# Kernel tuning notes

Hardware: AMD Instinct MI355X
Metric: run time of the kernel (lower is better)

## Reference

```python
import jax, jax.numpy as jnp
import numpy as np

NEG_SLOPE = 0.2


def gat_conv(x, edge_index, W, a_src, a_dst, b, concat):
    """PyG-style GATConv: add self-loops, linear, edge attention, scatter-softmax, scatter-add."""
    N = x.shape[0]
    H, C = a_src.shape
    loop = jnp.arange(N)
    src = jnp.concatenate([edge_index[0], loop])  # source j (messages flow j -> i)
    dst = jnp.concatenate([edge_index[1], loop])  # target i (aggregation node)
    h = (x @ W).reshape(N, H, C)                  # [N,H,C]
    alpha_s = jnp.sum(h * a_src, axis=-1)         # [N,H]
    alpha_d = jnp.sum(h * a_dst, axis=-1)         # [N,H]
    e = jax.nn.leaky_relu(alpha_s[src] + alpha_d[dst], NEG_SLOPE)  # [E,H]
    # numerically stable scatter-softmax over edges grouped by destination node
    m = jax.ops.segment_max(e, dst, num_segments=N)                # [N,H]
    ex = jnp.exp(e - m[dst])
    denom = jax.ops.segment_sum(ex, dst, num_segments=N)           # [N,H]
    alpha = ex / (denom[dst] + 1e-16)                              # [E,H]
    out = jax.ops.segment_sum(h[src] * alpha[:, :, None], dst, num_segments=N)  # [N,H,C]
    out = out.reshape(N, H * C) if concat else out.mean(axis=1)
    return out + b


def setup_inputs() -> dict:
    key = jax.random.key(0)
    ks = jax.random.split(key, 12)
    N, E, F_IN, HID, OUT, HEADS = 100000, 1600000, 128, 128, 64, 4
    C1 = HID // HEADS
    x = jax.random.normal(ks[0], (N, F_IN), dtype=jnp.float32)
    edge_index = jax.random.randint(ks[1], (2, E), 0, N, dtype=jnp.int64)
    s = 0.05
    return {
        "x": x,
        "edge_index": edge_index,
        "W1": jax.random.normal(ks[2], (F_IN, HEADS * C1), dtype=jnp.float32) * s,
        "a_src1": jax.random.normal(ks[3], (HEADS, C1), dtype=jnp.float32) * s,
        "a_dst1": jax.random.normal(ks[4], (HEADS, C1), dtype=jnp.float32) * s,
        "b1": jnp.zeros((HEADS * C1,), dtype=jnp.float32),
        "W2": jax.random.normal(ks[5], (HID, OUT), dtype=jnp.float32) * s,
        "a_src2": jax.random.normal(ks[6], (1, OUT), dtype=jnp.float32) * s,
        "a_dst2": jax.random.normal(ks[7], (1, OUT), dtype=jnp.float32) * s,
        "b2": jnp.zeros((OUT,), dtype=jnp.float32),
    }


def reference(x, edge_index, W1, a_src1, a_dst1, b1, W2, a_src2, a_dst2, b2):
    h = jax.nn.elu(gat_conv(x, edge_index, W1, a_src1, a_dst1, b1, concat=True))
    # F.dropout(p=0.5, training=False) is the identity in eval mode
    out = gat_conv(h, edge_index, W2, a_src2, a_dst2, b2, concat=False)
    return out
```

## Files before the change

kernel.cpp:

```cpp
#include <hip/hip_runtime.h>
#include <hip/hip_fp16.h>
#include <math.h>


#define BSH 9
#define DPB 512
#define NBK 256
#define CH1 16384
#define LOG2E 1.44269504088896f

__device__ __forceinline__ float exp2_fast(float x) {
#if __has_builtin(__builtin_amdgcn_exp2f)
    return __builtin_amdgcn_exp2f(x);
#else
    return exp2f(x);
#endif
}


__global__ __launch_bounds__(256) void bucket_hist(const int* __restrict__ ei, int E, int N,
                                                   unsigned* __restrict__ bcount) {
    __shared__ unsigned hist[NBK];
    int t = threadIdx.x;
    hist[t] = 0;
    __syncthreads();
    int Etot = E + N;
    for (int k = blockIdx.x * 256 + t; k < Etot; k += gridDim.x * 256) {
        int d = (k < E) ? ei[E + k] : (k - E);
        atomicAdd(&hist[d >> BSH], 1u);
    }
    __syncthreads();
    unsigned c = hist[t];
    if (c) atomicAdd(&bcount[t], c);
}

__global__ void scan_buckets(const unsigned* __restrict__ bcount, unsigned* __restrict__ bbase,
                             unsigned* __restrict__ bcursor) {
    __shared__ unsigned s[NBK];
    int t = threadIdx.x;
    unsigned v = bcount[t];
    s[t] = v;
    __syncthreads();
    for (int o = 1; o < NBK; o <<= 1) {
        unsigned add = (t >= o) ? s[t - o] : 0;
        __syncthreads();
        s[t] += add;
        __syncthreads();
    }
    unsigned excl = s[t] - v;
    bbase[t] = excl;
    bcursor[t] = excl;
    if (t == NBK - 1) bbase[NBK] = excl + v;
}

__global__ __launch_bounds__(256) void bucket_scatter(const int* __restrict__ ei, int E, int N,
                                                      unsigned* __restrict__ bcursor,
                                                      uint2* __restrict__ rec) {
    __shared__ unsigned hist[NBK];
    __shared__ unsigned base[NBK];
    int t = threadIdx.x;
    hist[t] = 0;
    __syncthreads();
    int Etot = E + N;
    int k0 = blockIdx.x * CH1;
    int k1 = min(k0 + CH1, Etot);
    for (int k = k0 + t; k < k1; k += 256) {
        int d = (k < E) ? ei[E + k] : (k - E);
        atomicAdd(&hist[d >> BSH], 1u);
    }
    __syncthreads();
    unsigned c = hist[t];
    base[t] = c ? atomicAdd(&bcursor[t], c) : 0u;
    hist[t] = 0;
    __syncthreads();
    for (int k = k0 + t; k < k1; k += 256) {
        int s, d;
        if (k < E) { s = ei[k]; d = ei[E + k]; } else { s = d = k - E; }
        int b = d >> BSH;
        unsigned r = atomicAdd(&hist[b], 1u);
        rec[base[b] + r] = make_uint2((unsigned)s, (unsigned)d);
    }
}

__global__ __launch_bounds__(256) void bucket_sort(const uint2* __restrict__ rec,
                                                   const unsigned* __restrict__ bbase,
                                                   int* __restrict__ offs, int* __restrict__ srcs,
                                                   int N, int Etot) {
    __shared__ unsigned hist[DPB];
    __shared__ unsigned tsum[256];
    int t = threadIdx.x, bb = blockIdx.x;
    unsigned r0 = bbase[bb], r1 = bbase[bb + 1];
    hist[t] = 0;
    hist[t + 256] = 0;
    __syncthreads();
    int dlo = bb << BSH;
    for (unsigned k = r0 + t; k < r1; k += 256) {
        uint2 e = rec[k];
        atomicAdd(&hist[e.y - dlo], 1u);
    }
    __syncthreads();
    unsigned h0 = hist[2 * t], h1 = hist[2 * t + 1];
    tsum[t] = h0 + h1;
    __syncthreads();
    for (int o = 1; o < 256; o <<= 1) {
        unsigned a = (t >= o) ? tsum[t - o] : 0;
        __syncthreads();
        tsum[t] += a;
        __syncthreads();
    }
    unsigned tb = tsum[t] - (h0 + h1);
    int d0 = dlo + 2 * t;
    if (d0 < N) offs[d0] = (int)(r0 + tb);
    if (d0 + 1 < N) offs[d0 + 1] = (int)(r0 + tb + h0);
    hist[2 * t] = tb;
    hist[2 * t + 1] = tb + h0;
    __syncthreads();
    for (unsigned k = r0 + t; k < r1; k += 256) {
        uint2 e = rec[k];
        unsigned r = atomicAdd(&hist[e.y - dlo], 1u);
        srcs[r0 + r] = (int)e.x;
    }
    if (bb == 0 && t == 0) offs[N] = Etot;
}


template <int NC, int H, typename InT, typename OutT>
__global__ __launch_bounds__(256) void gemm_k128(const InT* __restrict__ A,
                                                 const float* __restrict__ B,
                                                 OutT* __restrict__ C,
                                                 const float* __restrict__ a_src,
                                                 const float* __restrict__ a_dst,
                                                 float* __restrict__ as,
                                                 float* __restrict__ ad, int M) {
    constexpr int BM = 64, BK = 32, K = 128;
    constexpr int TPR = NC / 4;
    constexpr int R = BM / (256 / TPR);
    constexpr int TXH = TPR / H;
    __shared__ float AsT[BK][BM + 4];
    __shared__ float Bs[BK][NC];
    int tid = threadIdx.x;
    int tx = tid % TPR, ty = tid / TPR;
    int rowBase = blockIdx.x * BM;
    float acc[R][4] = {};
    for (int k0 = 0; k0 < K; k0 += BK) {
#pragma unroll
        for (int i = 0; i < 4; ++i) {
            int lin = tid + i * 256;
            int row = lin >> 4;
            int kp = lin & 15;
            int grow = rowBase + row;
            if (grow >= M) grow = M - 1;
            float2 v;
            if constexpr (sizeof(InT) == 2) {
                __half2 hv = *reinterpret_cast<const __half2*>((const __half*)A + (size_t)grow * K + k0 + kp * 2);
                v = __half22float2(hv);
            } else {
                v = *reinterpret_cast<const float2*>((const float*)A + (size_t)grow * K + k0 + kp * 2);
            }
            AsT[kp * 2][row] = v.x;
            AsT[kp * 2 + 1][row] = v.y;
        }
#pragma unroll
        for (int i = 0; i < (BK * NC) / 1024; ++i) {
            int lin = tid + i * 256;
            int row = lin / (NC / 4);
            int col4 = lin % (NC / 4);
            float4 v = *reinterpret_cast<const float4*>(B + (size_t)(k0 + row) * NC + col4 * 4);
            *reinterpret_cast<float4*>(&Bs[row][col4 * 4]) = v;
        }
        __syncthreads();
#pragma unroll
        for (int kk = 0; kk < BK; ++kk) {
            float4 bv = *reinterpret_cast<const float4*>(&Bs[kk][tx * 4]);
            float a[R];
#pragma unroll
            for (int r4 = 0; r4 < R; r4 += 4) {
                float4 av = *reinterpret_cast<const float4*>(&AsT[kk][ty * R + r4]);
                a[r4] = av.x; a[r4 + 1] = av.y; a[r4 + 2] = av.z; a[r4 + 3] = av.w;
            }
#pragma unroll
            for (int r = 0; r < R; ++r) {
                acc[r][0] = fmaf(a[r], bv.x, acc[r][0]);
                acc[r][1] = fmaf(a[r], bv.y, acc[r][1]);
                acc[r][2] = fmaf(a[r], bv.z, acc[r][2]);
                acc[r][3] = fmaf(a[r], bv.w, acc[r][3]);
            }
        }
        __syncthreads();
    }
    float4 asv = *reinterpret_cast<const float4*>(a_src + tx * 4);
    float4 adv = *reinterpret_cast<const float4*>(a_dst + tx * 4);
#pragma unroll
    for (int r = 0; r < R; ++r) {
        int grow = rowBase + ty * R + r;
        bool live = grow < M;
        if (live) {
            if constexpr (sizeof(OutT) == 2) {
                __half2 p0 = __floats2half2_rn(acc[r][0], acc[r][1]);
                __half2 p1 = __floats2half2_rn(acc[r][2], acc[r][3]);
                __half2* cp = reinterpret_cast<__half2*>((__half*)C + (size_t)grow * NC + tx * 4);
                cp[0] = p0;
                cp[1] = p1;
            } else {
                float4 v = make_float4(acc[r][0], acc[r][1], acc[r][2], acc[r][3]);
                *reinterpret_cast<float4*>((float*)C + (size_t)grow * NC + tx * 4) = v;
            }
        }
        float ps = acc[r][0] * asv.x + acc[r][1] * asv.y + acc[r][2] * asv.z + acc[r][3] * asv.w;
        float pd = acc[r][0] * adv.x + acc[r][1] * adv.y + acc[r][2] * adv.z + acc[r][3] * adv.w;
#pragma unroll
        for (int o = 1; o < TXH; o <<= 1) {
            ps += __shfl_xor(ps, o, 64);
            pd += __shfl_xor(pd, o, 64);
        }
        if ((tx & (TXH - 1)) == 0 && live) {
            int head = tx / TXH;
            as[(size_t)grow * H + head] = ps * LOG2E;
            ad[(size_t)grow * H + head] = pd * LOG2E;
        }
    }
}


__global__ __launch_bounds__(256) void aggregate1(const __half* __restrict__ h,
                                                  const float* __restrict__ as,
                                                  const float* __restrict__ ad,
                                                  const int* __restrict__ offs,
                                                  const int* __restrict__ srcs,
                                                  const float* __restrict__ bias,
                                                  __half* __restrict__ out, int N) {
    unsigned wid = (blockIdx.x * blockDim.x + threadIdx.x) >> 6;
    unsigned lane = threadIdx.x & 63;
    if (wid >= (unsigned)N) return;
    unsigned head = lane >> 4;
    float adv = ad[wid * 4u + head];
    int e0 = offs[wid], e1 = offs[wid + 1];
    int e1m1 = e1 - 1;
    const __half2* hp = reinterpret_cast<const __half2*>(h);
    float acc0 = 0.f, acc1 = 0.f, den = 0.f;
    for (int e = e0; e < e1; e += 4) {
        unsigned j0 = (unsigned)srcs[min(e, e1m1)];
        unsigned j1 = (unsigned)srcs[min(e + 1, e1m1)];
        unsigned j2 = (unsigned)srcs[min(e + 2, e1m1)];
        unsigned j3 = (unsigned)srcs[min(e + 3, e1m1)];
        float t0 = as[j0 * 4u + head] + adv;
        float t1 = as[j1 * 4u + head] + adv;
        float t2 = as[j2 * 4u + head] + adv;
        float t3 = as[j3 * 4u + head] + adv;
        __half2 h0 = hp[j0 * 64u + lane];
        __half2 h1 = hp[j1 * 64u + lane];
        __half2 h2 = hp[j2 * 64u + lane];
        __half2 h3 = hp[j3 * 64u + lane];
        float x0 = exp2_fast(fmaxf(t0, 0.2f * t0));
        float x1 = exp2_fast(fmaxf(t1, 0.2f * t1));
        float x2 = exp2_fast(fmaxf(t2, 0.2f * t2));
        float x3 = exp2_fast(fmaxf(t3, 0.2f * t3));
        x1 = (e + 1 < e1) ? x1 : 0.f;
        x2 = (e + 2 < e1) ? x2 : 0.f;
        x3 = (e + 3 < e1) ? x3 : 0.f;
        float2 f0 = __half22float2(h0), f1 = __half22float2(h1);
        float2 f2 = __half22float2(h2), f3 = __half22float2(h3);
        acc0 = fmaf(x0, f0.x, acc0); acc1 = fmaf(x0, f0.y, acc1);
        acc0 = fmaf(x1, f1.x, acc0); acc1 = fmaf(x1, f1.y, acc1);
        acc0 = fmaf(x2, f2.x, acc0); acc1 = fmaf(x2, f2.y, acc1);
        acc0 = fmaf(x3, f3.x, acc0); acc1 = fmaf(x3, f3.y, acc1);
        den += (x0 + x1) + (x2 + x3);
    }
    float r = 1.0f / (den + 1e-16f);
    float v0 = acc0 * r + bias[2 * lane];
    float v1 = acc1 * r + bias[2 * lane + 1];
    v0 = (v0 > 0.f) ? v0 : expm1f(v0);
    v1 = (v1 > 0.f) ? v1 : expm1f(v1);
    reinterpret_cast<__half2*>(out)[wid * 64u + lane] = __floats2half2_rn(v0, v1);
}

__global__ __launch_bounds__(256) void aggregate2(const __half* __restrict__ h,
                                                  const float* __restrict__ as,
                                                  const float* __restrict__ ad,
                                                  const int* __restrict__ offs,
                                                  const int* __restrict__ srcs,
                                                  const float* __restrict__ bias,
                                                  float* __restrict__ out, int N) {
    unsigned wid = (blockIdx.x * blockDim.x + threadIdx.x) >> 6;
    unsigned lane = threadIdx.x & 63;
    if (wid >= (unsigned)N) return;
    float adv = ad[wid];
    int e0 = offs[wid], e1 = offs[wid + 1];
    int e1m1 = e1 - 1;
    float acc = 0.f, den = 0.f;
    for (int e = e0; e < e1; e += 4) {
        unsigned j0 = (unsigned)srcs[min(e, e1m1)];
        unsigned j1 = (unsigned)srcs[min(e + 1, e1m1)];
        unsigned j2 = (unsigned)srcs[min(e + 2, e1m1)];
        unsigned j3 = (unsigned)srcs[min(e + 3, e1m1)];
        float t0 = as[j0] + adv;
        float t1 = as[j1] + adv;
        float t2 = as[j2] + adv;
        float t3 = as[j3] + adv;
        __half h0 = h[j0 * 64u + lane];
        __half h1 = h[j1 * 64u + lane];
        __half h2 = h[j2 * 64u + lane];
        __half h3 = h[j3 * 64u + lane];
        float x0 = exp2_fast(fmaxf(t0, 0.2f * t0));
        float x1 = exp2_fast(fmaxf(t1, 0.2f * t1));
        float x2 = exp2_fast(fmaxf(t2, 0.2f * t2));
        float x3 = exp2_fast(fmaxf(t3, 0.2f * t3));
        x1 = (e + 1 < e1) ? x1 : 0.f;
        x2 = (e + 2 < e1) ? x2 : 0.f;
        x3 = (e + 3 < e1) ? x3 : 0.f;
        acc = fmaf(x0, __half2float(h0), acc);
        acc = fmaf(x1, __half2float(h1), acc);
        acc = fmaf(x2, __half2float(h2), acc);
        acc = fmaf(x3, __half2float(h3), acc);
        den += (x0 + x1) + (x2 + x3);
    }
    float r = 1.0f / (den + 1e-16f);
    out[wid * 64u + lane] = acc * r + bias[lane];
}


extern "C" void kernel_launch(void* const* d_in, const int* in_sizes, int n_in,
                              void* d_out, int out_size, void* d_ws, size_t ws_size,
                              hipStream_t stream) {
    const float* x      = (const float*)d_in[0];
    const int*   ei     = (const int*)d_in[1];
    const float* W1     = (const float*)d_in[2];
    const float* a_src1 = (const float*)d_in[3];
    const float* a_dst1 = (const float*)d_in[4];
    const float* b1     = (const float*)d_in[5];
    const float* W2     = (const float*)d_in[6];
    const float* a_src2 = (const float*)d_in[7];
    const float* a_dst2 = (const float*)d_in[8];
    const float* b2     = (const float*)d_in[9];
    float* out = (float*)d_out;

    const int N = out_size / 64;
    const int E = in_sizes[1] / 2;
    const int Etot = E + N;

    size_t off = 0;
    auto carve = [&](size_t bytes) -> void* {
        void* p = (char*)d_ws + off;
        off += (bytes + 255) & ~(size_t)255;
        return p;
    };
    __half* h1      = (__half*)carve((size_t)N * 128 * 2);
    __half* hmid    = (__half*)carve((size_t)N * 128 * 2);
    float* as1      = (float*)carve((size_t)N * 4 * 4);
    float* ad1      = (float*)carve((size_t)N * 4 * 4);
    float* as2      = (float*)carve((size_t)N * 4);
    float* ad2      = (float*)carve((size_t)N * 4);
    int*   offs     = (int*)carve((size_t)(N + 1) * 4);
    int*   srcs     = (int*)carve((size_t)Etot * 4);
    uint2* rec      = (uint2*)carve((size_t)Etot * 8);
    unsigned* bcount  = (unsigned*)carve(NBK * 4);
    unsigned* bbase   = (unsigned*)carve((NBK + 1) * 4);
    unsigned* bcursor = (unsigned*)carve(NBK * 4);
    __half* h2      = h1;

    hipMemsetAsync(bcount, 0, NBK * sizeof(unsigned), stream);
    bucket_hist<<<128, 256, 0, stream>>>(ei, E, N, bcount);
    scan_buckets<<<1, 256, 0, stream>>>(bcount, bbase, bcursor);
    bucket_scatter<<<(Etot + CH1 - 1) / CH1, 256, 0, stream>>>(ei, E, N, bcursor, rec);
    bucket_sort<<<(N + DPB - 1) / DPB, 256, 0, stream>>>(rec, bbase, offs, srcs, N, Etot);

    gemm_k128<128, 4, float, __half><<<(N + 63) / 64, 256, 0, stream>>>(
        x, W1, h1, a_src1, a_dst1, as1, ad1, N);
    aggregate1<<<(N + 3) / 4, 256, 0, stream>>>(h1, as1, ad1, offs, srcs, b1, hmid, N);

    gemm_k128<64, 1, __half, __half><<<(N + 63) / 64, 256, 0, stream>>>(
        hmid, W2, h2, a_src2, a_dst2, as2, ad2, N);
    aggregate2<<<(N + 3) / 4, 256, 0, stream>>>(h2, as2, ad2, offs, srcs, b2, out, N);
}
```

Before: 407.6 us.

## Process four destination nodes per wave with wide vector gathers in aggregation

Merges the two aggregation kernels into one templated kernel in which each 16-lane quarter-wave handles one destination node. Each lane loads 16 or 8 bytes of the source feature row and accumulates several channels, in place of one whole wave per node with 2- or 4-byte loads. The aim is fewer, wider memory transactions and more nodes in flight per wave. The cost is load imbalance: every node's loop runs to the maximum degree among the four nodes sharing a wave, and the edge unroll drops from 4 to 2.

```diff
diff --git a/kernel.cpp b/kernel.cpp
--- a/kernel.cpp
+++ b/kernel.cpp
@@ -1,6 +1,7 @@
 #include <hip/hip_runtime.h>
 #include <hip/hip_fp16.h>
 #include <math.h>
+#include <string.h>
 
 
 #define BSH 9
@@ -222,100 +223,104 @@
 }
 
 
-__global__ __launch_bounds__(256) void aggregate1(const __half* __restrict__ h,
+template <int H, int F, bool DOELU, typename OutT>
+__global__ __launch_bounds__(256) void aggregateQ(const __half* __restrict__ h,
                                                   const float* __restrict__ as,
                                                   const float* __restrict__ ad,
                                                   const int* __restrict__ offs,
                                                   const int* __restrict__ srcs,
                                                   const float* __restrict__ bias,
-                                                  __half* __restrict__ out, int N) {
-    unsigned wid = (blockIdx.x * blockDim.x + threadIdx.x) >> 6;
+                                                  OutT* __restrict__ out, int N) {
+    constexpr int CPL = F / 16;
+    constexpr int NH2 = CPL / 2;
+    unsigned wave = (blockIdx.x * blockDim.x + threadIdx.x) >> 6;
     unsigned lane = threadIdx.x & 63;
-    if (wid >= (unsigned)N) return;
-    unsigned head = lane >> 4;
-    float adv = ad[wid * 4u + head];
-    int e0 = offs[wid], e1 = offs[wid + 1];
-    int e1m1 = e1 - 1;
-    const __half2* hp = reinterpret_cast<const __half2*>(h);
-    float acc0 = 0.f, acc1 = 0.f, den = 0.f;
-    for (int e = e0; e < e1; e += 4) {
-        unsigned j0 = (unsigned)srcs[min(e, e1m1)];
-        unsigned j1 = (unsigned)srcs[min(e + 1, e1m1)];
-        unsigned j2 = (unsigned)srcs[min(e + 2, e1m1)];
-        unsigned j3 = (unsigned)srcs[min(e + 3, e1m1)];
-        float t0 = as[j0 * 4u + head] + adv;
-        float t1 = as[j1 * 4u + head] + adv;
-        float t2 = as[j2 * 4u + head] + adv;
-        float t3 = as[j3 * 4u + head] + adv;
-        __half2 h0 = hp[j0 * 64u + lane];
-        __half2 h1 = hp[j1 * 64u + lane];
-        __half2 h2 = hp[j2 * 64u + lane];
-        __half2 h3 = hp[j3 * 64u + lane];
-        float x0 = exp2_fast(fmaxf(t0, 0.2f * t0));
-        float x1 = exp2_fast(fmaxf(t1, 0.2f * t1));
-        float x2 = exp2_fast(fmaxf(t2, 0.2f * t2));
-        float x3 = exp2_fast(fmaxf(t3, 0.2f * t3));
-        x1 = (e + 1 < e1) ? x1 : 0.f;
-        x2 = (e + 2 < e1) ? x2 : 0.f;
-        x3 = (e + 3 < e1) ? x3 : 0.f;
-        float2 f0 = __half22float2(h0), f1 = __half22float2(h1);
-        float2 f2 = __half22float2(h2), f3 = __half22float2(h3);
-        acc0 = fmaf(x0, f0.x, acc0); acc1 = fmaf(x0, f0.y, acc1);
-        acc0 = fmaf(x1, f1.x, acc0); acc1 = fmaf(x1, f1.y, acc1);
-        acc0 = fmaf(x2, f2.x, acc0); acc1 = fmaf(x2, f2.y, acc1);
-        acc0 = fmaf(x3, f3.x, acc0); acc1 = fmaf(x3, f3.y, acc1);
-        den += (x0 + x1) + (x2 + x3);
+    unsigned lig = lane & 15;
+    unsigned node = wave * 4u + (lane >> 4);
+    bool live = node < (unsigned)N;
+    unsigned nc = live ? node : (unsigned)(N - 1);
+    unsigned head = (lig * CPL) / (F / H);
+    float adv = ad[nc * H + head];
+    int e0 = offs[nc], e1 = offs[nc + 1];
+    int deg = e1 - e0, e1m1 = e1 - 1;
+    int md = deg;
+    md = max(md, __shfl_xor(md, 16, 64));
+    md = max(md, __shfl_xor(md, 32, 64));
+    float2 acc[NH2] = {};
+    float den = 0.f;
+    for (int k = 0; k < md; k += 2) {
+        unsigned ja = (unsigned)srcs[min(e0 + k, e1m1)];
+        unsigned jb = (unsigned)srcs[min(e0 + k + 1, e1m1)];
+        float ta = as[ja * H + head] + adv;
+        float tb = as[jb * H + head] + adv;
+        __half2 ha[NH2], hb[NH2];
+        if constexpr (NH2 == 4) {
+            uint4 va = *reinterpret_cast<const uint4*>(h + ja * (unsigned)F + lig * CPL);
+            uint4 vb = *reinterpret_cast<const uint4*>(h + jb * (unsigned)F + lig * CPL);
+            memcpy(ha, &va, 16);
+            memcpy(hb, &vb, 16);
+        } else {
+            uint2 va = *reinterpret_cast<const uint2*>(h + ja * (unsigned)F + lig * CPL);
+            uint2 vb = *reinterpret_cast<const uint2*>(h + jb * (unsigned)F + lig * CPL);
+            memcpy(ha, &va, 8);
+            memcpy(hb, &vb, 8);
+        }
+        float xa = exp2_fast(fmaxf(ta, 0.2f * ta));
+        float xb = exp2_fast(fmaxf(tb, 0.2f * tb));
+        xa = (k < deg) ? xa : 0.f;
+        xb = (k + 1 < deg) ? xb : 0.f;
+#pragma unroll
+        for (int q = 0; q < NH2; ++q) {
+            float2 fa = __half22float2(ha[q]);
+            float2 fb = __half22float2(hb[q]);
+            acc[q].x = fmaf(xa, fa.x, acc[q].x);
+            acc[q].y = fmaf(xa, fa.y, acc[q].y);
+            acc[q].x = fmaf(xb, fb.x, acc[q].x);
+            acc[q].y = fmaf(xb, fb.y, acc[q].y);
+        }
+        den += xa + xb;
     }
     float r = 1.0f / (den + 1e-16f);
-    float v0 = acc0 * r + bias[2 * lane];
-    float v1 = acc1 * r + bias[2 * lane + 1];
-    v0 = (v0 > 0.f) ? v0 : expm1f(v0);
-    v1 = (v1 > 0.f) ? v1 : expm1f(v1);
-    reinterpret_cast<__half2*>(out)[wid * 64u + lane] = __floats2half2_rn(v0, v1);
-}
-
-__global__ __launch_bounds__(256) void aggregate2(const __half* __restrict__ h,
-                                                  const float* __restrict__ as,
-                                                  const float* __restrict__ ad,
-                                                  const int* __restrict__ offs,
-                                                  const int* __restrict__ srcs,
-                                                  const float* __restrict__ bias,
-                                                  float* __restrict__ out, int N) {
-    unsigned wid = (blockIdx.x * blockDim.x + threadIdx.x) >> 6;
-    unsigned lane = threadIdx.x & 63;
-    if (wid >= (unsigned)N) return;
-    float adv = ad[wid];
-    int e0 = offs[wid], e1 = offs[wid + 1];
-    int e1m1 = e1 - 1;
-    float acc = 0.f, den = 0.f;
-    for (int e = e0; e < e1; e += 4) {
-        unsigned j0 = (unsigned)srcs[min(e, e1m1)];
-        unsigned j1 = (unsigned)srcs[min(e + 1, e1m1)];
-        unsigned j2 = (unsigned)srcs[min(e + 2, e1m1)];
-        unsigned j3 = (unsigned)srcs[min(e + 3, e1m1)];
-        float t0 = as[j0] + adv;
-        float t1 = as[j1] + adv;
-        float t2 = as[j2] + adv;
-        float t3 = as[j3] + adv;
-        __half h0 = h[j0 * 64u + lane];
-        __half h1 = h[j1 * 64u + lane];
-        __half h2 = h[j2 * 64u + lane];
-        __half h3 = h[j3 * 64u + lane];
-        float x0 = exp2_fast(fmaxf(t0, 0.2f * t0));
-        float x1 = exp2_fast(fmaxf(t1, 0.2f * t1));
-        float x2 = exp2_fast(fmaxf(t2, 0.2f * t2));
-        float x3 = exp2_fast(fmaxf(t3, 0.2f * t3));
-        x1 = (e + 1 < e1) ? x1 : 0.f;
-        x2 = (e + 2 < e1) ? x2 : 0.f;
-        x3 = (e + 3 < e1) ? x3 : 0.f;
-        acc = fmaf(x0, __half2float(h0), acc);
-        acc = fmaf(x1, __half2float(h1), acc);
-        acc = fmaf(x2, __half2float(h2), acc);
-        acc = fmaf(x3, __half2float(h3), acc);
-        den += (x0 + x1) + (x2 + x3);
-    }
-    float r = 1.0f / (den + 1e-16f);
-    out[wid * 64u + lane] = acc * r + bias[lane];
+    if (!live) return;
+    const float* bp = bias + lig * CPL;
+    if constexpr (sizeof(OutT) == 2) {
+        __half2 st[NH2];
+#pragma unroll
+        for (int q = 0; q < NH2; ++q) {
+            float v0 = acc[q].x * r + bp[2 * q];
+            float v1 = acc[q].y * r + bp[2 * q + 1];
+            if constexpr (DOELU) {
+                v0 = (v0 > 0.f) ? v0 : expm1f(v0);
+                v1 = (v1 > 0.f) ? v1 : expm1f(v1);
+            }
+            st[q] = __floats2half2_rn(v0, v1);
+        }
+        if constexpr (NH2 == 4) {
+            uint4 v; memcpy(&v, st, 16);
+            *reinterpret_cast<uint4*>((__half*)out + node * (unsigned)F + lig * CPL) = v;
+        } else {
+            uint2 v; memcpy(&v, st, 8);
+            *reinterpret_cast<uint2*>((__half*)out + node * (unsigned)F + lig * CPL) = v;
+        }
+    } else {
+        float vs[CPL];
+#pragma unroll
+        for (int q = 0; q < NH2; ++q) {
+            float v0 = acc[q].x * r + bp[2 * q];
+            float v1 = acc[q].y * r + bp[2 * q + 1];
+            if constexpr (DOELU) {
+                v0 = (v0 > 0.f) ? v0 : expm1f(v0);
+                v1 = (v1 > 0.f) ? v1 : expm1f(v1);
+            }
+            vs[2 * q] = v0;
+            vs[2 * q + 1] = v1;
+        }
+#pragma unroll
+        for (int q4 = 0; q4 < CPL; q4 += 4) {
+            float4 v = make_float4(vs[q4], vs[q4 + 1], vs[q4 + 2], vs[q4 + 3]);
+            *reinterpret_cast<float4*>((float*)out + node * (unsigned)F + lig * CPL + q4) = v;
+        }
+    }
 }
 
 
@@ -366,9 +371,11 @@
 
     gemm_k128<128, 4, float, __half><<<(N + 63) / 64, 256, 0, stream>>>(
         x, W1, h1, a_src1, a_dst1, as1, ad1, N);
-    aggregate1<<<(N + 3) / 4, 256, 0, stream>>>(h1, as1, ad1, offs, srcs, b1, hmid, N);
+    aggregateQ<4, 128, true, __half><<<(N + 15) / 16, 256, 0, stream>>>(
+        h1, as1, ad1, offs, srcs, b1, hmid, N);
 
     gemm_k128<64, 1, __half, __half><<<(N + 63) / 64, 256, 0, stream>>>(
         hmid, W2, h2, a_src2, a_dst2, as2, ad2, N);
-    aggregate2<<<(N + 3) / 4, 256, 0, stream>>>(h2, as2, ad2, offs, srcs, b2, out, N);
-}
+    aggregateQ<1, 64, false, float><<<(N + 15) / 16, 256, 0, stream>>>(
+        h2, as2, ad2, offs, srcs, b2, out, N);
+}
```

Result: faster. 390.0 us (-4.3%).
